# Optimization experiments

Measured on AMD Instinct MI355X. Metric: run time of the kernel, lower is better.

## Reference

```python
import jax, jax.numpy as jnp
import numpy as np

H = 8          # num_heads
D = 64         # out_dim per head
ROT = D // 2   # rotary dim per spatial axis (out_dim // relative_emb_dim)
MIN_FREQ = 1.0 / 64


def _freqs(t):
    # t: (bs, N) coordinates -> (bs, N, ROT)
    inv_freq = 1.0 / (10000.0 ** (jnp.arange(0, ROT, 2, dtype=jnp.float32) / ROT))
    f = (t / MIN_FREQ)[..., None] * inv_freq  # (bs, N, ROT/2)
    return jnp.concatenate([f, f], axis=-1)   # (bs, N, ROT)


def _rotate_half(x):
    x1, x2 = jnp.split(x, 2, axis=-1)
    return jnp.concatenate([-x2, x1], axis=-1)


def _rope(t, f):
    return t * jnp.cos(f) + _rotate_half(t) * jnp.sin(f)


def reference(h, pos, Wq, Wk, Wv, src, dst):
    bs, N, _ = pos.shape
    hb = h.reshape(bs, N, -1)                       # (bs, N, C)
    # Faithful to torch: Linear output (bs,N,H*D) .view(bs,H,N,D) is a raw
    # memory reinterpretation, i.e. a reshape, not a transpose.
    Qh = (hb @ Wq.T).reshape(bs, H, N, D)
    Kh = (hb @ Wk.T).reshape(bs, H, N, D)
    Vh = (hb @ Wv.T).reshape(bs, H, N, D)

    fx = _freqs(pos[..., 0])[:, None]               # (bs, 1, N, ROT) broadcast over heads
    fy = _freqs(pos[..., 1])[:, None]

    def rope2d(t):
        return jnp.concatenate([_rope(t[..., :ROT], fx), _rope(t[..., ROT:], fy)], axis=-1)

    Qh = rope2d(Qh)
    Kh = rope2d(Kh)

    Qn = Qh.reshape(-1, H, D)                       # (bs*N, H, D) flat node layout
    Kn = Kh.reshape(-1, H, D)
    Vn = Vh.reshape(-1, H, D)

    # edge attention: gather, dot, clamped exp, scatter-sum
    score = jnp.sum(Kn[src] * Qn[dst], axis=-1)     # (E, H)
    score = jnp.exp(jnp.clip(score / np.sqrt(D).astype(np.float32), -5.0, 5.0))

    nseg = bs * N
    wV = jax.ops.segment_sum(Vn[src] * score[..., None], dst, num_segments=nseg)  # (nseg,H,D)
    z = jax.ops.segment_sum(score, dst, num_segments=nseg)                        # (nseg,H)

    attn_out = wV / z[..., None]
    return attn_out.reshape(-1, H * D)


def setup_inputs() -> dict:
    key = jax.random.key(0)
    k = jax.random.split(key, 7)
    bs, N, C, E = 4, 4096, 256, 524288
    return {
        "h": jax.random.normal(k[0], (bs * N, C), dtype=jnp.float32),
        "pos": jax.random.uniform(k[1], (bs, N, 2), dtype=jnp.float32),
        "Wq": jax.random.normal(k[2], (H * D, C), dtype=jnp.float32) * 0.05,
        "Wk": jax.random.normal(k[3], (H * D, C), dtype=jnp.float32) * 0.05,
        "Wv": jax.random.normal(k[4], (H * D, C), dtype=jnp.float32) * 0.05,
        "src": jax.random.randint(k[5], (E,), 0, bs * N, dtype=jnp.int32),
        "dst": jax.random.randint(k[6], (E,), 0, bs * N, dtype=jnp.int32),
    }
```

## Files before the change

kernel.cpp:

```cpp
#include <hip/hip_runtime.h>
#include <math.h>

#define NODES 16384
#define CIN   256
#define HD    512
#define NPOS  4096
#define NHEAD 8
#define DDIM  64
#define HN    (NODES * CIN)
#define WN    (HD * CIN)

typedef float f32x4 __attribute__((ext_vector_type(4)));
typedef unsigned int u32x4 __attribute__((ext_vector_type(4)));
typedef short s16x8 __attribute__((ext_vector_type(8)));

__device__ inline unsigned short f2bf(float f) {
  unsigned int u = __float_as_uint(f);
  u += 0x7fffu + ((u >> 16) & 1u);
  return (unsigned short)(u >> 16);
}

__global__ __launch_bounds__(256) void conv_hist_kernel(
    const float* __restrict__ h, const float* __restrict__ wq,
    const float* __restrict__ wk, const float* __restrict__ wv,
    unsigned short* __restrict__ out,
    const int* __restrict__ dst, int* __restrict__ count, int E) {
  int t = blockIdx.x * 256 + threadIdx.x;
  if (t < E) atomicAdd(&count[dst[t]], 1);

  size_t e = (size_t)t * 8;
  const float* s;
  size_t off;
  if (e < HN)               { s = h;  off = e; }
  else if (e < HN + WN)     { s = wq; off = e - HN; }
  else if (e < HN + 2 * WN) { s = wk; off = e - HN - WN; }
  else                      { s = wv; off = e - HN - 2 * WN; }
  float4 f0 = *(const float4*)(s + off);
  float4 f1 = *(const float4*)(s + off + 4);
  u32x4 o;
  o[0] = f2bf(f0.x) | ((unsigned int)f2bf(f0.y) << 16);
  o[1] = f2bf(f0.z) | ((unsigned int)f2bf(f0.w) << 16);
  o[2] = f2bf(f1.x) | ((unsigned int)f2bf(f1.y) << 16);
  o[3] = f2bf(f1.z) | ((unsigned int)f2bf(f1.w) << 16);
  *(u32x4*)(out + e) = o;
}

__global__ __launch_bounds__(256) void gemm_mfma_kernel(
    const unsigned short* __restrict__ hb,
    const unsigned short* __restrict__ wb,
    const float* __restrict__ pos,
    unsigned short* __restrict__ Qb, unsigned short* __restrict__ Kb,
    unsigned short* __restrict__ Vb) {
  const int z = blockIdx.z;
  const unsigned short* B = wb + (size_t)z * WN;
  unsigned short* C = z == 0 ? Qb : (z == 1 ? Kb : Vb);

  __shared__ __align__(16) unsigned short As[2][128 * 32];
  __shared__ __align__(16) unsigned short Bs[2][128 * 32];

  const int tid = threadIdx.x;
  const int lane = tid & 63, w = tid >> 6;
  const int row0 = blockIdx.y * 128, col0 = blockIdx.x * 128;
  const int wr = w >> 1, wc = w & 1;

  const int r_l = lane >> 2;
  const int kc = (lane & 3) * 8;

  f32x4 acc[4][4] = {};

#define STAGE(bufi, kt)                                                        \
  {                                                                            \
    _Pragma("unroll") for (int u = 0; u < 2; ++u) {                            \
      int blk = u * 4 + w;                                                     \
      int r = blk * 16 + r_l;                                                  \
      __builtin_amdgcn_global_load_lds(                                        \
          (const __attribute__((address_space(1))) void*)(hb +                 \
              (size_t)(row0 + r) * CIN + (kt) + kc),                           \
          (__attribute__((address_space(3))) void*)(&As[bufi][blk * 512]),     \
          16, 0, 0);                                                           \
      __builtin_amdgcn_global_load_lds(                                        \
          (const __attribute__((address_space(1))) void*)(B +                  \
              (size_t)(col0 + r) * CIN + (kt) + kc),                           \
          (__attribute__((address_space(3))) void*)(&Bs[bufi][blk * 512]),     \
          16, 0, 0);                                                           \
    }                                                                          \
  }

  STAGE(0, 0);
  __syncthreads();

  int cur = 0;
  for (int t = 0; t < 8; ++t) {
    if (t < 7) STAGE(cur ^ 1, (t + 1) * 32);

    s16x8 af[4], bfr[4];
#pragma unroll
    for (int mi = 0; mi < 4; ++mi)
      af[mi] = *(const s16x8*)(&As[cur][(wr * 64 + mi * 16 + (lane & 15)) * 32 + (lane >> 4) * 8]);
#pragma unroll
    for (int ni = 0; ni < 4; ++ni)
      bfr[ni] = *(const s16x8*)(&Bs[cur][(wc * 64 + ni * 16 + (lane & 15)) * 32 + (lane >> 4) * 8]);
#pragma unroll
    for (int mi = 0; mi < 4; ++mi)
#pragma unroll
      for (int ni = 0; ni < 4; ++ni)
        acc[mi][ni] = __builtin_amdgcn_mfma_f32_16x16x32_bf16(
            af[mi], bfr[ni], acc[mi][ni], 0, 0, 0);

    __syncthreads();
    cur ^= 1;
  }
#undef STAGE

  const int head = blockIdx.x * 2 + wc;
  const int cb = col0 + wc * 64 + (lane & 15);
  const float invf = exp2f(-(float)(lane & 15) * 0.83048202372184f);

#pragma unroll
  for (int mi = 0; mi < 4; ++mi) {
#pragma unroll
    for (int r = 0; r < 4; ++r) {
      int row = row0 + wr * 64 + mi * 16 + (lane >> 4) * 4 + r;
      float v0 = acc[mi][0][r], v1 = acc[mi][1][r];
      float v2 = acc[mi][2][r], v3 = acc[mi][3][r];
      if (z < 2) {
        int b = row >> 12;
        int rem = ((row & 4095) << 3) + head;
        int n = rem & (NPOS - 1);
        const float* pp = pos + ((size_t)((b << 12) + n)) * 2;
        float a0 = pp[0] * 64.0f * invf;
        float a1 = pp[1] * 64.0f * invf;
        float s0, c0, s1, c1;
        sincosf(a0, &s0, &c0);
        sincosf(a1, &s1, &c1);
        float nx0 = v0 * c0 - v1 * s0;
        float nx1 = v1 * c0 + v0 * s0;
        float ny0 = v2 * c1 - v3 * s1;
        float ny1 = v3 * c1 + v2 * s1;
        v0 = nx0; v1 = nx1; v2 = ny0; v3 = ny1;
      }
      unsigned short* cp = C + (size_t)row * HD + cb;
      cp[0]  = f2bf(v0);
      cp[16] = f2bf(v1);
      cp[32] = f2bf(v2);
      cp[48] = f2bf(v3);
    }
  }
}

__global__ __launch_bounds__(256) void scan_kernel(
    const int* __restrict__ count, int* __restrict__ offset,
    int* __restrict__ cursor) {
  __shared__ int psum[256];
  __shared__ int pref[256];
  int t = threadIdx.x;
  int base = t * (NODES / 256);
  int s = 0;
  for (int i = 0; i < NODES / 256; ++i) s += count[base + i];
  psum[t] = s;
  __syncthreads();
  if (t == 0) {
    int run = 0;
    for (int i = 0; i < 256; ++i) { pref[i] = run; run += psum[i]; }
  }
  __syncthreads();
  int off = pref[t];
  for (int i = 0; i < NODES / 256; ++i) {
    int c = count[base + i];
    offset[base + i] = off;
    cursor[base + i] = off;
    off += c;
  }
  if (t == 255) offset[NODES] = off;
}

__global__ __launch_bounds__(256) void scatter_kernel(
    const int* __restrict__ src, const int* __restrict__ dst,
    int* __restrict__ cursor, int* __restrict__ srcs, int E) {
  int t = blockIdx.x * 256 + threadIdx.x;
  if (t < E) {
    int p = atomicAdd(&cursor[dst[t]], 1);
    srcs[p] = src[t];
  }
}

__global__ __launch_bounds__(256) void node_kernel(
    const unsigned short* __restrict__ Qb, const unsigned short* __restrict__ Kb,
    const unsigned short* __restrict__ Vb,
    const int* __restrict__ srcs, const int* __restrict__ offset,
    float* __restrict__ out) {
  __shared__ float wv[4][HD];
  __shared__ float zb[4][NHEAD];
  const int n = blockIdx.x;
  const int tid = threadIdx.x;
  const int lane = tid & 63, w = tid >> 6;
  const int hh = lane >> 3, g = lane & 7;

  const int beg = offset[n], end = offset[n + 1];

  u32x4 qu = *(const u32x4*)(Qb + (size_t)n * HD + lane * 8);
  float qf[8];
#pragma unroll
  for (int j = 0; j < 4; ++j) {
    qf[2 * j]     = __uint_as_float(qu[j] << 16);
    qf[2 * j + 1] = __uint_as_float(qu[j] & 0xffff0000u);
  }

  float a[8] = {0, 0, 0, 0, 0, 0, 0, 0};
  float zacc = 0.f;

  for (int i = beg + w; i < end; i += 4) {
    int s = srcs[i];
    u32x4 ku = *(const u32x4*)(Kb + (size_t)s * HD + lane * 8);
    u32x4 vu = *(const u32x4*)(Vb + (size_t)s * HD + lane * 8);
    float dot = 0.f;
#pragma unroll
    for (int j = 0; j < 4; ++j) {
      dot += __uint_as_float(ku[j] << 16) * qf[2 * j];
      dot += __uint_as_float(ku[j] & 0xffff0000u) * qf[2 * j + 1];
    }
    dot += __shfl_xor(dot, 1);
    dot += __shfl_xor(dot, 2);
    dot += __shfl_xor(dot, 4);
    float sc = expf(fminf(fmaxf(dot * 0.125f, -5.0f), 5.0f));
#pragma unroll
    for (int j = 0; j < 4; ++j) {
      a[2 * j]     += __uint_as_float(vu[j] << 16) * sc;
      a[2 * j + 1] += __uint_as_float(vu[j] & 0xffff0000u) * sc;
    }
    zacc += sc;
  }

  *(float4*)&wv[w][lane * 8]     = make_float4(a[0], a[1], a[2], a[3]);
  *(float4*)&wv[w][lane * 8 + 4] = make_float4(a[4], a[5], a[6], a[7]);
  if (g == 0) zb[w][hh] = zacc;
  __syncthreads();

  const int d0 = tid * 2;
  float r0 = wv[0][d0] + wv[1][d0] + wv[2][d0] + wv[3][d0];
  float r1 = wv[0][d0 + 1] + wv[1][d0 + 1] + wv[2][d0 + 1] + wv[3][d0 + 1];
  const int head = d0 >> 6;
  float zz = zb[0][head] + zb[1][head] + zb[2][head] + zb[3][head];
  float inv = 1.0f / zz;
  *(float2*)&out[(size_t)n * HD + d0] = make_float2(r0 * inv, r1 * inv);
}

extern "C" void kernel_launch(void* const* d_in, const int* in_sizes, int n_in,
                              void* d_out, int out_size, void* d_ws,
                              size_t ws_size, hipStream_t stream) {
  const float* h   = (const float*)d_in[0];
  const float* pos = (const float*)d_in[1];
  const float* Wq  = (const float*)d_in[2];
  const float* Wk  = (const float*)d_in[3];
  const float* Wv  = (const float*)d_in[4];
  const int* src   = (const int*)d_in[5];
  const int* dst   = (const int*)d_in[6];
  const int E = in_sizes[5];

  unsigned short* hb  = (unsigned short*)d_ws;
  unsigned short* wb  = hb + HN;
  unsigned short* Qb  = wb + 3 * WN;
  unsigned short* Kb  = Qb + (size_t)NODES * HD;
  unsigned short* Vb  = Kb + (size_t)NODES * HD;
  int* count  = (int*)(Vb + (size_t)NODES * HD);
  int* offset = count + NODES;
  int* cursor = offset + NODES + 1;
  int* srcs   = cursor + NODES;
  float* out = (float*)d_out;

  hipMemsetAsync(count, 0, NODES * sizeof(int), stream);

  conv_hist_kernel<<<(HN + 3 * WN) / 8 / 256, 256, 0, stream>>>(
      h, Wq, Wk, Wv, hb, dst, count, E);

  scan_kernel<<<1, 256, 0, stream>>>(count, offset, cursor);
  scatter_kernel<<<(E + 255) / 256, 256, 0, stream>>>(src, dst, cursor, srcs, E);

  gemm_mfma_kernel<<<dim3(HD / 128, NODES / 128, 3), 256, 0, stream>>>(
      hb, wb, pos, Qb, Kb, Vb);

  node_kernel<<<NODES, 256, 0, stream>>>(Qb, Kb, Vb, srcs, offset, out);
}
```

Before: 308.0 us.

## Record per-edge rank in histogram pass to drop second atomic scatter

The histogram atomic now returns each edge's rank within its destination bucket and stores it, so the CSR placement pass becomes a plain indexed write with no atomics. The cursor array goes away. The single-block scan replaces its serial prefix over 256 partial sums with a wave shuffle scan. The node kernel also switches expf to the fast __expf intrinsic. In exchange there is an extra E-sized rank buffer to write and read back.

New measurement: 284.5 us. 7.6% less time.

```diff
diff --git a/kernel.cpp b/kernel.cpp
--- a/kernel.cpp
+++ b/kernel.cpp
@@ -20,13 +20,14 @@
   return (unsigned short)(u >> 16);
 }
 
-__global__ __launch_bounds__(256) void conv_hist_kernel(
+__global__ __launch_bounds__(256) void conv_rank_kernel(
     const float* __restrict__ h, const float* __restrict__ wq,
     const float* __restrict__ wk, const float* __restrict__ wv,
     unsigned short* __restrict__ out,
-    const int* __restrict__ dst, int* __restrict__ count, int E) {
+    const int* __restrict__ dst, int* __restrict__ count,
+    int* __restrict__ rank, int E) {
   int t = blockIdx.x * 256 + threadIdx.x;
-  if (t < E) atomicAdd(&count[dst[t]], 1);
+  if (t < E) rank[t] = atomicAdd(&count[dst[t]], 1);
 
   size_t e = (size_t)t * 8;
   const float* s;
@@ -43,6 +44,49 @@
   o[2] = f2bf(f1.x) | ((unsigned int)f2bf(f1.y) << 16);
   o[3] = f2bf(f1.z) | ((unsigned int)f2bf(f1.w) << 16);
   *(u32x4*)(out + e) = o;
+}
+
+__global__ __launch_bounds__(256) void scan_kernel(
+    const int* __restrict__ count, int* __restrict__ offset) {
+  __shared__ int psum[256];
+  __shared__ int pref[256];
+  int t = threadIdx.x;
+  int base = t * (NODES / 256);
+  int s = 0;
+  for (int i = 0; i < NODES / 256; ++i) s += count[base + i];
+  psum[t] = s;
+  __syncthreads();
+  if (t < 64) {
+    int a0 = psum[4 * t], a1 = psum[4 * t + 1];
+    int a2 = psum[4 * t + 2], a3 = psum[4 * t + 3];
+    int loc = a0 + a1 + a2 + a3;
+    int sc = loc;
+#pragma unroll
+    for (int d = 1; d < 64; d <<= 1) {
+      int v = __shfl_up(sc, d);
+      if (t >= d) sc += v;
+    }
+    int excl = sc - loc;
+    pref[4 * t]     = excl;
+    pref[4 * t + 1] = excl + a0;
+    pref[4 * t + 2] = excl + a0 + a1;
+    pref[4 * t + 3] = excl + a0 + a1 + a2;
+  }
+  __syncthreads();
+  int off = pref[t];
+  for (int i = 0; i < NODES / 256; ++i) {
+    offset[base + i] = off;
+    off += count[base + i];
+  }
+  if (t == 255) offset[NODES] = off;
+}
+
+__global__ __launch_bounds__(256) void place_kernel(
+    const int* __restrict__ src, const int* __restrict__ dst,
+    const int* __restrict__ offset, const int* __restrict__ rank,
+    int* __restrict__ srcs, int E) {
+  int t = blockIdx.x * 256 + threadIdx.x;
+  if (t < E) srcs[offset[dst[t]] + rank[t]] = src[t];
 }
 
 __global__ __launch_bounds__(256) void gemm_mfma_kernel(
@@ -148,42 +192,6 @@
   }
 }
 
-__global__ __launch_bounds__(256) void scan_kernel(
-    const int* __restrict__ count, int* __restrict__ offset,
-    int* __restrict__ cursor) {
-  __shared__ int psum[256];
-  __shared__ int pref[256];
-  int t = threadIdx.x;
-  int base = t * (NODES / 256);
-  int s = 0;
-  for (int i = 0; i < NODES / 256; ++i) s += count[base + i];
-  psum[t] = s;
-  __syncthreads();
-  if (t == 0) {
-    int run = 0;
-    for (int i = 0; i < 256; ++i) { pref[i] = run; run += psum[i]; }
-  }
-  __syncthreads();
-  int off = pref[t];
-  for (int i = 0; i < NODES / 256; ++i) {
-    int c = count[base + i];
-    offset[base + i] = off;
-    cursor[base + i] = off;
-    off += c;
-  }
-  if (t == 255) offset[NODES] = off;
-}
-
-__global__ __launch_bounds__(256) void scatter_kernel(
-    const int* __restrict__ src, const int* __restrict__ dst,
-    int* __restrict__ cursor, int* __restrict__ srcs, int E) {
-  int t = blockIdx.x * 256 + threadIdx.x;
-  if (t < E) {
-    int p = atomicAdd(&cursor[dst[t]], 1);
-    srcs[p] = src[t];
-  }
-}
-
 __global__ __launch_bounds__(256) void node_kernel(
     const unsigned short* __restrict__ Qb, const unsigned short* __restrict__ Kb,
     const unsigned short* __restrict__ Vb,
@@ -222,7 +230,7 @@
     dot += __shfl_xor(dot, 1);
     dot += __shfl_xor(dot, 2);
     dot += __shfl_xor(dot, 4);
-    float sc = expf(fminf(fmaxf(dot * 0.125f, -5.0f), 5.0f));
+    float sc = __expf(fminf(fmaxf(dot * 0.125f, -5.0f), 5.0f));
 #pragma unroll
     for (int j = 0; j < 4; ++j) {
       a[2 * j]     += __uint_as_float(vu[j] << 16) * sc;
@@ -264,17 +272,18 @@
   unsigned short* Vb  = Kb + (size_t)NODES * HD;
   int* count  = (int*)(Vb + (size_t)NODES * HD);
   int* offset = count + NODES;
-  int* cursor = offset + NODES + 1;
-  int* srcs   = cursor + NODES;
+  int* rank   = offset + NODES + 1;
+  int* srcs   = rank + E;
   float* out = (float*)d_out;
 
   hipMemsetAsync(count, 0, NODES * sizeof(int), stream);
 
-  conv_hist_kernel<<<(HN + 3 * WN) / 8 / 256, 256, 0, stream>>>(
-      h, Wq, Wk, Wv, hb, dst, count, E);
-
-  scan_kernel<<<1, 256, 0, stream>>>(count, offset, cursor);
-  scatter_kernel<<<(E + 255) / 256, 256, 0, stream>>>(src, dst, cursor, srcs, E);
+  conv_rank_kernel<<<(HN + 3 * WN) / 8 / 256, 256, 0, stream>>>(
+      h, Wq, Wk, Wv, hb, dst, count, rank, E);
+
+  scan_kernel<<<1, 256, 0, stream>>>(count, offset);
+  place_kernel<<<(E + 255) / 256, 256, 0, stream>>>(
+      src, dst, offset, rank, srcs, E);
 
   gemm_mfma_kernel<<<dim3(HD / 128, NODES / 128, 3), 256, 0, stream>>>(
       hb, wb, pos, Qb, Kb, Vb);
```
